# Performance work log

Hardware: AMD Instinct MI355X
Metric: run time of the kernel (lower is better)

The kernel has to match this reference:

```python
import jax, jax.numpy as jnp
import numpy as np

N_SPK, M_UTT, D_EMB = 1024, 32, 512


def setup_inputs() -> dict:
    key = jax.random.key(0)
    k0, = jax.random.split(key, 1)
    embeddings = jax.random.normal(k0, (N_SPK, M_UTT, D_EMB), dtype=jnp.float32)
    return {
        "embeddings": embeddings,
        "w": jnp.asarray(5.0, dtype=jnp.float32),
        "b": jnp.asarray(1.0, dtype=jnp.float32),
        "N": N_SPK,
        "M": M_UTT,
    }


def reference(embeddings, w, b, N, M):
    # embeddings: [N, M, D]
    centroids = embeddings.mean(axis=1)          # [N, D]
    sum_ = embeddings.sum(axis=1)                # [N, D]
    e_flat = embeddings.reshape(N * M, -1)       # [NM, D]
    cosine_sim = e_flat @ centroids.T            # [NM, N]

    # Exclusive-centroid diagonal overwrite (faithful to source, including
    # the operator precedence: c_j = sum_[j] - e[j,k] / (1 - M)):
    #   diag[j,k] = (sum_[j] - e[j,k]/(1-M)) . e[j,k]
    inv = 1.0 / (1.0 - M)
    diag = (jnp.einsum('nmd,nd->nm', embeddings, sum_)
            - inv * jnp.sum(embeddings * embeddings, axis=-1))  # [N, M]

    rows = jnp.arange(N * M)
    cols = jnp.repeat(jnp.arange(N), M)          # label layout: [0]*M, [1]*M, ...
    cosine_sim = cosine_sim.at[rows, cols].set(diag.reshape(-1))

    logits = w * cosine_sim + b                  # [NM, N]
    # cross_entropy with labels = cols, mean reduction
    logz = jax.nn.logsumexp(logits, axis=-1)     # [NM]
    loss = jnp.mean(logz - logits[rows, cols])
    return loss
```

## Files before the change

kernel.cpp:

```cpp
#include <hip/hip_runtime.h>

#define N_SPK 1024
#define M_UTT 32
#define D_EMB 512
#define NROWS (N_SPK * M_UTT)

#define NEG_INF (-__builtin_inff())
#define MARGIN 25.0f

using f32x4 = __attribute__((ext_vector_type(4))) float;


__global__ __launch_bounds__(256)
void prep_kernel(const float* __restrict__ e,
                 float* __restrict__ sumf, float* __restrict__ ssqA,
                 float* __restrict__ dgl, float* __restrict__ c2A,
                 const float* __restrict__ wp, const float* __restrict__ bp,
                 float* __restrict__ out, int* __restrict__ count,
                 int* __restrict__ doneCnt) {
    __shared__ float csum[4][D_EMB];
    __shared__ float c2red[4];
    const int n = blockIdx.x;
    const int wv = threadIdx.x >> 6, l = threadIdx.x & 63;

    if (n == 0 && threadIdx.x == 0) { out[0] = 0.f; *count = 0; *doneCnt = 0; }

    float xs[8][8];
    float ssq[8];
    float cacc[8];
#pragma unroll
    for (int j = 0; j < 8; ++j) cacc[j] = 0.f;

#pragma unroll
    for (int mi = 0; mi < 8; ++mi) {
        const int m = mi * 4 + wv;
        const size_t row = (size_t)n * M_UTT + m;
        const float* p = e + row * D_EMB + l * 8;
        float4 x0 = *(const float4*)p;
        float4 x1 = *(const float4*)(p + 4);
        xs[mi][0] = x0.x; xs[mi][1] = x0.y; xs[mi][2] = x0.z; xs[mi][3] = x0.w;
        xs[mi][4] = x1.x; xs[mi][5] = x1.y; xs[mi][6] = x1.z; xs[mi][7] = x1.w;
        float sq = 0.f;
#pragma unroll
        for (int j = 0; j < 8; ++j) {
            float x = xs[mi][j];
            cacc[j] += x;
            sq = __builtin_fmaf(x, x, sq);
        }
#pragma unroll
        for (int off = 32; off; off >>= 1) sq += __shfl_xor(sq, off);
        ssq[mi] = sq;
        if (l == 0) ssqA[row] = sq;
    }

#pragma unroll
    for (int j = 0; j < 8; ++j) csum[wv][l * 8 + j] = cacc[j];
    __syncthreads();
    float c2acc = 0.f;
    for (int d = threadIdx.x; d < D_EMB; d += 256) {
        float s = csum[0][d] + csum[1][d] + csum[2][d] + csum[3][d];
        csum[0][d] = s;
        sumf[(size_t)n * D_EMB + d] = s;
        float c = s * (1.0f / M_UTT);
        c2acc = __builtin_fmaf(c, c, c2acc);
    }
#pragma unroll
    for (int off = 32; off; off >>= 1) c2acc += __shfl_xor(c2acc, off);
    if (l == 0) c2red[wv] = c2acc;
    __syncthreads();
    if (threadIdx.x == 0)
        c2A[n] = (c2red[0] + c2red[1]) + (c2red[2] + c2red[3]);

    float sv[8];
#pragma unroll
    for (int j = 0; j < 8; ++j) sv[j] = csum[0][l * 8 + j];
    const float w = wp[0], bb = bp[0];
#pragma unroll
    for (int mi = 0; mi < 8; ++mi) {
        float dg = 0.f;
#pragma unroll
        for (int j = 0; j < 8; ++j) dg = __builtin_fmaf(xs[mi][j], sv[j], dg);
#pragma unroll
        for (int off = 32; off; off >>= 1) dg += __shfl_xor(dg, off);
        if (l == 0) {
            const size_t row = (size_t)n * M_UTT + mi * 4 + wv;
            dgl[row] = __builtin_fmaf(w, dg + ssq[mi] * (1.0f / 31.0f), bb);
        }
    }
}

__global__ __launch_bounds__(256)
void select_kernel(const float* __restrict__ ssqA, const float* __restrict__ dgl,
                   const float* __restrict__ c2A,
                   const float* __restrict__ wp, const float* __restrict__ bp,
                   int* __restrict__ count, int* __restrict__ active) {
    __shared__ float red[4];
    float m = 0.f;
#pragma unroll
    for (int i = 0; i < 4; ++i)
        m = fmaxf(m, c2A[threadIdx.x + i * 256]);
#pragma unroll
    for (int off = 32; off; off >>= 1) m = fmaxf(m, __shfl_xor(m, off));
    if ((threadIdx.x & 63) == 0) red[threadIdx.x >> 6] = m;
    __syncthreads();
    const float c2 = fmaxf(fmaxf(red[0], red[1]), fmaxf(red[2], red[3]));
    const float Cmax = __builtin_sqrtf(c2);

    const int row = blockIdx.x * 256 + threadIdx.x;
    const float bound = __builtin_fmaf(
        __builtin_fabsf(wp[0]) * __builtin_sqrtf(ssqA[row]), Cmax, bp[0]);
    if (dgl[row] - bound < MARGIN) {
        int slot = atomicAdd(count, 1);
        active[slot] = row;
    }
}

__global__ __launch_bounds__(64)
void active_kernel(const float* __restrict__ e, const float* __restrict__ sumf,
                   const float* __restrict__ dgl,
                   const int* __restrict__ count, const int* __restrict__ active,
                   const float* __restrict__ wp, const float* __restrict__ bp,
                   float2* __restrict__ pm16, int* __restrict__ doneCnt,
                   float* __restrict__ out) {
    __shared__ float er[D_EMB];
    __shared__ int lastFlag;
    const int tid = threadIdx.x;
    const int cnt = *count;
    if (cnt == 0) return;
    const float w = wp[0], bb = bp[0];

    const int g16 = blockIdx.x & 15;
    const int slot0 = blockIdx.x >> 4;
    const int gstride = gridDim.x >> 4;

    if (tid == 0) lastFlag = 0;
    int myItems = 0;

    for (int slot = slot0; slot < cnt; slot += gstride) {
        const int row = active[slot];
        __syncthreads();
#pragma unroll
        for (int i = 0; i < 8; ++i)
            er[tid + i * 64] = e[(size_t)row * D_EMB + tid + i * 64];
        __syncthreads();

        const int j = g16 * 64 + tid;
        const float* sp = sumf + (size_t)j * D_EMB;
        float d0 = 0.f, d1 = 0.f, d2 = 0.f, d3 = 0.f;
        for (int k = 0; k < D_EMB; k += 4) {
            float4 s4 = *(const float4*)(sp + k);
            d0 = __builtin_fmaf(er[k + 0], s4.x, d0);
            d1 = __builtin_fmaf(er[k + 1], s4.y, d1);
            d2 = __builtin_fmaf(er[k + 2], s4.z, d2);
            d3 = __builtin_fmaf(er[k + 3], s4.w, d3);
        }
        const float dot = (d0 + d1) + (d2 + d3);
        float lg = __builtin_fmaf(w, dot * (1.0f / M_UTT), bb);
        if (j == (row >> 5)) lg = dgl[row];

        float mx = lg;
#pragma unroll
        for (int off = 32; off; off >>= 1) mx = fmaxf(mx, __shfl_xor(mx, off));
        float ss = __expf(lg - mx);
#pragma unroll
        for (int off = 32; off; off >>= 1) ss += __shfl_xor(ss, off);
        if (tid == 0) {
            float2 v; v.x = mx; v.y = ss;
            __hip_atomic_store((unsigned long long*)&pm16[slot * 16 + g16],
                               __builtin_bit_cast(unsigned long long, v),
                               __ATOMIC_RELAXED, __HIP_MEMORY_SCOPE_AGENT);
        }
        ++myItems;
    }

    __syncthreads();
    if (tid == 0 && myItems > 0) {
        int old = __hip_atomic_fetch_add(doneCnt, myItems,
                                         __ATOMIC_ACQ_REL,
                                         __HIP_MEMORY_SCOPE_AGENT);
        if (old + myItems == cnt * 16) lastFlag = 1;
    }
    __syncthreads();

    if (lastFlag) {
        for (int slot = tid; slot < cnt; slot += 64) {
            float2 pm[4];
#pragma unroll
            for (int c = 0; c < 4; ++c) {
                float2 r0, r1, r2, r3;
                unsigned long long b0 = __hip_atomic_load(
                    (unsigned long long*)&pm16[slot * 16 + 4 * c + 0],
                    __ATOMIC_RELAXED, __HIP_MEMORY_SCOPE_AGENT);
                unsigned long long b1 = __hip_atomic_load(
                    (unsigned long long*)&pm16[slot * 16 + 4 * c + 1],
                    __ATOMIC_RELAXED, __HIP_MEMORY_SCOPE_AGENT);
                unsigned long long b2 = __hip_atomic_load(
                    (unsigned long long*)&pm16[slot * 16 + 4 * c + 2],
                    __ATOMIC_RELAXED, __HIP_MEMORY_SCOPE_AGENT);
                unsigned long long b3 = __hip_atomic_load(
                    (unsigned long long*)&pm16[slot * 16 + 4 * c + 3],
                    __ATOMIC_RELAXED, __HIP_MEMORY_SCOPE_AGENT);
                r0 = __builtin_bit_cast(float2, b0);
                r1 = __builtin_bit_cast(float2, b1);
                r2 = __builtin_bit_cast(float2, b2);
                r3 = __builtin_bit_cast(float2, b3);
                float M = fmaxf(fmaxf(r0.x, r1.x), fmaxf(r2.x, r3.x));
                float S = r0.y * __expf(r0.x - M)
                        + r1.y * __expf(r1.x - M)
                        + r2.y * __expf(r2.x - M)
                        + r3.y * __expf(r3.x - M);
                pm[c].x = M; pm[c].y = S;
            }
            float M = fmaxf(fmaxf(pm[0].x, pm[1].x), fmaxf(pm[2].x, pm[3].x));
            float S = pm[0].y * __expf(pm[0].x - M) + pm[1].y * __expf(pm[1].x - M)
                    + pm[2].y * __expf(pm[2].x - M) + pm[3].y * __expf(pm[3].x - M);
            float loss = M + __logf(S) - dgl[active[slot]];
            atomicAdd(out, loss * (1.0f / NROWS));
        }
    }
}


__global__ void centroid_kernel(const float* __restrict__ e,
                                float* __restrict__ cent) {
    int gid = blockIdx.x * 256 + threadIdx.x;
    int n = gid >> 9;
    int d = gid & 511;
    const float* p = e + ((size_t)n * M_UTT) * D_EMB + d;
    float s = 0.f;
#pragma unroll
    for (int m = 0; m < M_UTT; ++m) s += p[(size_t)m * D_EMB];
    cent[gid] = s * (1.0f / M_UTT);
}

__global__ void normsq_kernel(const float* __restrict__ e,
                              float* __restrict__ nsq) {
    int wv = threadIdx.x >> 6;
    int lane = threadIdx.x & 63;
    int row = blockIdx.x * 4 + wv;
    const float* p = e + (size_t)row * D_EMB + lane;
    float s = 0.f;
#pragma unroll
    for (int j = 0; j < 8; ++j) { float x = p[j * 64]; s += x * x; }
#pragma unroll
    for (int off = 32; off; off >>= 1) s += __shfl_xor(s, off);
    if (lane == 0) nsq[row] = s;
}

#define BR 64
#define BC 128
#define BK 16
#define TR 4
#define TC 8

__global__ __launch_bounds__(256, 2)
void ge2e_main(const float* __restrict__ e, const float* __restrict__ cent,
               const float* __restrict__ nsq, const float* __restrict__ wp,
               const float* __restrict__ bp, float* __restrict__ partials) {
    __shared__ float As[BK][BR];
    __shared__ float Bs[BK][BC];
    __shared__ float diagLs[BR];
    __shared__ float red[16];

    const int tid = threadIdx.x;
    const int tx = tid & 15;
    const int ty = tid >> 4;
    const int blk = blockIdx.x;
    const int r0 = blk * BR;

    const float w = *wp;
    const float bb = *bp;

    float m_run[TR], s_run[TR];
#pragma unroll
    for (int i = 0; i < TR; ++i) { m_run[i] = NEG_INF; s_run[i] = 0.f; }

    const int a_row = tid >> 2;
    const int a_k   = (tid & 3) * 4;
    const int b_col = tid >> 1;
    const int b_k   = (tid & 1) * 8;

    for (int ct = 0; ct < N_SPK / BC; ++ct) {
        const int c0 = ct * BC;
        float acc[TR][TC];
#pragma unroll
        for (int i = 0; i < TR; ++i)
#pragma unroll
            for (int j = 0; j < TC; ++j) acc[i][j] = 0.f;

        for (int kk = 0; kk < D_EMB; kk += BK) {
            __syncthreads();
            {
                float4 av = *(const float4*)(e + (size_t)(r0 + a_row) * D_EMB + kk + a_k);
                As[a_k + 0][a_row] = av.x;
                As[a_k + 1][a_row] = av.y;
                As[a_k + 2][a_row] = av.z;
                As[a_k + 3][a_row] = av.w;
            }
            {
                const float* bp0 = cent + (size_t)(c0 + b_col) * D_EMB + kk + b_k;
                float4 bv0 = *(const float4*)(bp0);
                float4 bv1 = *(const float4*)(bp0 + 4);
                Bs[b_k + 0][b_col] = bv0.x;
                Bs[b_k + 1][b_col] = bv0.y;
                Bs[b_k + 2][b_col] = bv0.z;
                Bs[b_k + 3][b_col] = bv0.w;
                Bs[b_k + 4][b_col] = bv1.x;
                Bs[b_k + 5][b_col] = bv1.y;
                Bs[b_k + 6][b_col] = bv1.z;
                Bs[b_k + 7][b_col] = bv1.w;
            }
            __syncthreads();

#pragma unroll
            for (int k = 0; k < BK; ++k) {
                float4 a4 = *(const float4*)&As[k][ty * TR];
                float4 b4a = *(const float4*)&Bs[k][tx * TC];
                float4 b4b = *(const float4*)&Bs[k][tx * TC + 4];
                float av[TR] = {a4.x, a4.y, a4.z, a4.w};
                float bv[TC] = {b4a.x, b4a.y, b4a.z, b4a.w,
                                b4b.x, b4b.y, b4b.z, b4b.w};
#pragma unroll
                for (int i = 0; i < TR; ++i)
#pragma unroll
                    for (int j = 0; j < TC; ++j)
                        acc[i][j] = __builtin_fmaf(av[i], bv[j], acc[i][j]);
            }
        }

#pragma unroll
        for (int i = 0; i < TR; ++i) {
            const int grow = r0 + ty * TR + i;
            const int dcol = grow >> 5;
            float lv[TC];
#pragma unroll
            for (int j = 0; j < TC; ++j) {
                const int gcol = c0 + tx * TC + j;
                float v = acc[i][j];
                float lg;
                if (gcol == dcol) {
                    lg = __builtin_fmaf(w, __builtin_fmaf(32.0f, v,
                             (1.0f / 31.0f) * nsq[grow]), bb);
                    diagLs[ty * TR + i] = lg;
                } else {
                    lg = __builtin_fmaf(w, v, bb);
                }
                lv[j] = lg;
            }
            float mx = lv[0];
#pragma unroll
            for (int j = 1; j < TC; ++j) mx = fmaxf(mx, lv[j]);
#pragma unroll
            for (int off = 8; off; off >>= 1) mx = fmaxf(mx, __shfl_xor(mx, off));
            float ss = 0.f;
#pragma unroll
            for (int j = 0; j < TC; ++j) ss += __expf(lv[j] - mx);
#pragma unroll
            for (int off = 8; off; off >>= 1) ss += __shfl_xor(ss, off);
            float nm = fmaxf(m_run[i], mx);
            s_run[i] = s_run[i] * __expf(m_run[i] - nm) + ss * __expf(mx - nm);
            m_run[i] = nm;
        }
    }

    __syncthreads();
    if (tx == 0) {
        float part = 0.f;
#pragma unroll
        for (int i = 0; i < TR; ++i) {
            const int lr = ty * TR + i;
            part += m_run[i] + __logf(s_run[i]) - diagLs[lr];
        }
        red[ty] = part;
    }
    __syncthreads();
    if (tid == 0) {
        float t = 0.f;
#pragma unroll
        for (int i = 0; i < 16; ++i) t += red[i];
        partials[blk] = t;
    }
}

__global__ void reduce_kernel(const float* __restrict__ partials,
                              float* __restrict__ out) {
    __shared__ float red[4];
    int tid = threadIdx.x;
    float v = partials[tid] + partials[tid + 256];
#pragma unroll
    for (int off = 32; off; off >>= 1) v += __shfl_xor(v, off);
    if ((tid & 63) == 0) red[tid >> 6] = v;
    __syncthreads();
    if (tid == 0)
        out[0] = (red[0] + red[1] + red[2] + red[3]) * (1.0f / NROWS);
}


extern "C" void kernel_launch(void* const* d_in, const int* in_sizes, int n_in,
                              void* d_out, int out_size, void* d_ws, size_t ws_size,
                              hipStream_t stream) {
    const float* e  = (const float*)d_in[0];
    const float* wp = (const float*)d_in[1];
    const float* bp = (const float*)d_in[2];
    float* out = (float*)d_out;

    const size_t NEED_FAST = 6688776ull;

    if (ws_size >= NEED_FAST) {
        char* base = (char*)d_ws;
        float*  sumf    = (float*) (base);
        float*  ssqA    = (float*) (base + 2097152ull);
        float*  dgl     = (float*) (base + 2228224ull);
        int*    active  = (int*)   (base + 2359296ull);
        float2* pm16    = (float2*)(base + 2490368ull);
        float*  c2A     = (float*) (base + 6684672ull);
        int*    count   = (int*)   (base + 6688768ull);
        int*    doneCnt = (int*)   (base + 6688772ull);

        prep_kernel<<<N_SPK, 256, 0, stream>>>(e, sumf, ssqA, dgl, c2A,
                                               wp, bp, out, count, doneCnt);
        select_kernel<<<NROWS / 256, 256, 0, stream>>>(ssqA, dgl, c2A,
                                                       wp, bp, count, active);
        active_kernel<<<1024, 64, 0, stream>>>(e, sumf, dgl, count, active,
                                               wp, bp, pm16, doneCnt, out);
    } else {
        float* ws = (float*)d_ws;
        float* cent     = ws;
        float* nsq      = ws + 524288;
        float* partials = ws + 524288 + 32768;

        centroid_kernel<<<N_SPK * D_EMB / 256, 256, 0, stream>>>(e, cent);
        normsq_kernel<<<NROWS / 4, 256, 0, stream>>>(e, nsq);
        ge2e_main<<<NROWS / BR, 256, 0, stream>>>(e, cent, nsq, wp, bp, partials);
        reduce_kernel<<<1, 256, 0, stream>>>(partials, out);
    }
}
```

Before: 118.0 us.

## Fuse row selection into active-row logsumexp kernel, indexing partials by row

Removes the separate select kernel. Each active-kernel block now computes the centroid-norm bound itself and ballots over a fixed range of 512 rows, then processes the active rows inline. Partial max/sum results are stored per row instead of per compacted slot. Completion is detected with a per-block counter rather than an item count. This drops one launch and the serial dependency on the global active count, but work is assigned statically by row position, so blocks can be imbalanced if active rows cluster.

Measured after the change: 130.9 us. 11.0% more time.

```diff
diff --git a/kernel.cpp b/kernel.cpp
--- a/kernel.cpp
+++ b/kernel.cpp
@@ -17,13 +17,13 @@
                  float* __restrict__ dgl, float* __restrict__ c2A,
                  const float* __restrict__ wp, const float* __restrict__ bp,
                  float* __restrict__ out, int* __restrict__ count,
-                 int* __restrict__ doneCnt) {
+                 int* __restrict__ blocksDone) {
     __shared__ float csum[4][D_EMB];
     __shared__ float c2red[4];
     const int n = blockIdx.x;
     const int wv = threadIdx.x >> 6, l = threadIdx.x & 63;
 
-    if (n == 0 && threadIdx.x == 0) { out[0] = 0.f; *count = 0; *doneCnt = 0; }
+    if (n == 0 && threadIdx.x == 0) { out[0] = 0.f; *count = 0; *blocksDone = 0; }
 
     float xs[8][8];
     float ssq[8];
@@ -89,132 +89,128 @@
     }
 }
 
-__global__ __launch_bounds__(256)
-void select_kernel(const float* __restrict__ ssqA, const float* __restrict__ dgl,
-                   const float* __restrict__ c2A,
-                   const float* __restrict__ wp, const float* __restrict__ bp,
-                   int* __restrict__ count, int* __restrict__ active) {
-    __shared__ float red[4];
-    float m = 0.f;
-#pragma unroll
-    for (int i = 0; i < 4; ++i)
-        m = fmaxf(m, c2A[threadIdx.x + i * 256]);
-#pragma unroll
-    for (int off = 32; off; off >>= 1) m = fmaxf(m, __shfl_xor(m, off));
-    if ((threadIdx.x & 63) == 0) red[threadIdx.x >> 6] = m;
-    __syncthreads();
-    const float c2 = fmaxf(fmaxf(red[0], red[1]), fmaxf(red[2], red[3]));
-    const float Cmax = __builtin_sqrtf(c2);
-
-    const int row = blockIdx.x * 256 + threadIdx.x;
-    const float bound = __builtin_fmaf(
-        __builtin_fabsf(wp[0]) * __builtin_sqrtf(ssqA[row]), Cmax, bp[0]);
-    if (dgl[row] - bound < MARGIN) {
-        int slot = atomicAdd(count, 1);
-        active[slot] = row;
-    }
-}
-
 __global__ __launch_bounds__(64)
-void active_kernel(const float* __restrict__ e, const float* __restrict__ sumf,
-                   const float* __restrict__ dgl,
-                   const int* __restrict__ count, const int* __restrict__ active,
-                   const float* __restrict__ wp, const float* __restrict__ bp,
-                   float2* __restrict__ pm16, int* __restrict__ doneCnt,
-                   float* __restrict__ out) {
+void act2_kernel(const float* __restrict__ e, const float* __restrict__ sumf,
+                 const float* __restrict__ ssqA, const float* __restrict__ dgl,
+                 const float* __restrict__ c2A,
+                 const float* __restrict__ wp, const float* __restrict__ bp,
+                 int* __restrict__ count, int* __restrict__ active,
+                 float2* __restrict__ pm16, int* __restrict__ blocksDone,
+                 float* __restrict__ out) {
     __shared__ float er[D_EMB];
     __shared__ int lastFlag;
     const int tid = threadIdx.x;
-    const int cnt = *count;
-    if (cnt == 0) return;
+    const int g16 = blockIdx.x & 15;
+    const int r0 = (blockIdx.x >> 4) * 512;
     const float w = wp[0], bb = bp[0];
 
-    const int g16 = blockIdx.x & 15;
-    const int slot0 = blockIdx.x >> 4;
-    const int gstride = gridDim.x >> 4;
-
-    if (tid == 0) lastFlag = 0;
-    int myItems = 0;
-
-    for (int slot = slot0; slot < cnt; slot += gstride) {
-        const int row = active[slot];
-        __syncthreads();
-#pragma unroll
-        for (int i = 0; i < 8; ++i)
-            er[tid + i * 64] = e[(size_t)row * D_EMB + tid + i * 64];
-        __syncthreads();
-
-        const int j = g16 * 64 + tid;
-        const float* sp = sumf + (size_t)j * D_EMB;
-        float d0 = 0.f, d1 = 0.f, d2 = 0.f, d3 = 0.f;
-        for (int k = 0; k < D_EMB; k += 4) {
-            float4 s4 = *(const float4*)(sp + k);
-            d0 = __builtin_fmaf(er[k + 0], s4.x, d0);
-            d1 = __builtin_fmaf(er[k + 1], s4.y, d1);
-            d2 = __builtin_fmaf(er[k + 2], s4.z, d2);
-            d3 = __builtin_fmaf(er[k + 3], s4.w, d3);
-        }
-        const float dot = (d0 + d1) + (d2 + d3);
-        float lg = __builtin_fmaf(w, dot * (1.0f / M_UTT), bb);
-        if (j == (row >> 5)) lg = dgl[row];
-
-        float mx = lg;
-#pragma unroll
-        for (int off = 32; off; off >>= 1) mx = fmaxf(mx, __shfl_xor(mx, off));
-        float ss = __expf(lg - mx);
-#pragma unroll
-        for (int off = 32; off; off >>= 1) ss += __shfl_xor(ss, off);
-        if (tid == 0) {
-            float2 v; v.x = mx; v.y = ss;
-            __hip_atomic_store((unsigned long long*)&pm16[slot * 16 + g16],
-                               __builtin_bit_cast(unsigned long long, v),
-                               __ATOMIC_RELAXED, __HIP_MEMORY_SCOPE_AGENT);
-        }
-        ++myItems;
-    }
-
-    __syncthreads();
-    if (tid == 0 && myItems > 0) {
-        int old = __hip_atomic_fetch_add(doneCnt, myItems,
-                                         __ATOMIC_ACQ_REL,
+    float m = 0.f;
+#pragma unroll
+    for (int i = 0; i < 16; ++i) m = fmaxf(m, c2A[tid + i * 64]);
+#pragma unroll
+    for (int off = 32; off; off >>= 1) m = fmaxf(m, __shfl_xor(m, off));
+    const float Cmax = __builtin_sqrtf(m);
+    const float aw = __builtin_fabsf(w);
+
+    for (int i = 0; i < 8; ++i) {
+        const int row = r0 + i * 64 + tid;
+        const float bound = __builtin_fmaf(
+            aw * __builtin_sqrtf(ssqA[row]), Cmax, bb);
+        unsigned long long mask = __ballot(dgl[row] - bound < MARGIN);
+        while (mask) {
+            const int bit = __builtin_ctzll(mask);
+            mask &= mask - 1;
+            const int srow = r0 + i * 64 + bit;
+
+            {
+                const float4* src = (const float4*)(e + (size_t)srow * D_EMB);
+                ((float4*)er)[tid * 2]     = src[tid * 2];
+                ((float4*)er)[tid * 2 + 1] = src[tid * 2 + 1];
+            }
+            __syncthreads();
+
+            const int j = g16 * 64 + tid;
+            const float* sp = sumf + (size_t)j * D_EMB;
+            float d0 = 0.f, d1 = 0.f, d2 = 0.f, d3 = 0.f;
+            for (int k = 0; k < D_EMB; k += 4) {
+                float4 s4 = *(const float4*)(sp + k);
+                d0 = __builtin_fmaf(er[k + 0], s4.x, d0);
+                d1 = __builtin_fmaf(er[k + 1], s4.y, d1);
+                d2 = __builtin_fmaf(er[k + 2], s4.z, d2);
+                d3 = __builtin_fmaf(er[k + 3], s4.w, d3);
+            }
+            const float dot = (d0 + d1) + (d2 + d3);
+            float lg = __builtin_fmaf(w, dot * (1.0f / M_UTT), bb);
+            if (j == (srow >> 5)) lg = dgl[srow];
+
+            float mx = lg;
+#pragma unroll
+            for (int off = 32; off; off >>= 1)
+                mx = fmaxf(mx, __shfl_xor(mx, off));
+            float ss = __expf(lg - mx);
+#pragma unroll
+            for (int off = 32; off; off >>= 1) ss += __shfl_xor(ss, off);
+
+            if (tid == 0) {
+                float2 v; v.x = mx; v.y = ss;
+                __hip_atomic_store(
+                    (unsigned long long*)&pm16[(size_t)srow * 16 + g16],
+                    __builtin_bit_cast(unsigned long long, v),
+                    __ATOMIC_RELAXED, __HIP_MEMORY_SCOPE_AGENT);
+                if (g16 == 0) {
+                    int slot = atomicAdd(count, 1);
+                    __hip_atomic_store(&active[slot], srow,
+                                       __ATOMIC_RELAXED,
+                                       __HIP_MEMORY_SCOPE_AGENT);
+                }
+            }
+            __syncthreads();
+        }
+    }
+
+    if (tid == 0) {
+        int old = __hip_atomic_fetch_add(blocksDone, 1, __ATOMIC_ACQ_REL,
                                          __HIP_MEMORY_SCOPE_AGENT);
-        if (old + myItems == cnt * 16) lastFlag = 1;
+        lastFlag = (old == (int)(gridDim.x) - 1);
     }
     __syncthreads();
 
     if (lastFlag) {
+        const int cnt = __hip_atomic_load(count, __ATOMIC_RELAXED,
+                                          __HIP_MEMORY_SCOPE_AGENT);
         for (int slot = tid; slot < cnt; slot += 64) {
+            const int row = __hip_atomic_load(&active[slot], __ATOMIC_RELAXED,
+                                              __HIP_MEMORY_SCOPE_AGENT);
             float2 pm[4];
 #pragma unroll
             for (int c = 0; c < 4; ++c) {
-                float2 r0, r1, r2, r3;
                 unsigned long long b0 = __hip_atomic_load(
-                    (unsigned long long*)&pm16[slot * 16 + 4 * c + 0],
+                    (unsigned long long*)&pm16[(size_t)row * 16 + 4 * c + 0],
                     __ATOMIC_RELAXED, __HIP_MEMORY_SCOPE_AGENT);
                 unsigned long long b1 = __hip_atomic_load(
-                    (unsigned long long*)&pm16[slot * 16 + 4 * c + 1],
+                    (unsigned long long*)&pm16[(size_t)row * 16 + 4 * c + 1],
                     __ATOMIC_RELAXED, __HIP_MEMORY_SCOPE_AGENT);
                 unsigned long long b2 = __hip_atomic_load(
-                    (unsigned long long*)&pm16[slot * 16 + 4 * c + 2],
+                    (unsigned long long*)&pm16[(size_t)row * 16 + 4 * c + 2],
                     __ATOMIC_RELAXED, __HIP_MEMORY_SCOPE_AGENT);
                 unsigned long long b3 = __hip_atomic_load(
-                    (unsigned long long*)&pm16[slot * 16 + 4 * c + 3],
+                    (unsigned long long*)&pm16[(size_t)row * 16 + 4 * c + 3],
                     __ATOMIC_RELAXED, __HIP_MEMORY_SCOPE_AGENT);
-                r0 = __builtin_bit_cast(float2, b0);
-                r1 = __builtin_bit_cast(float2, b1);
-                r2 = __builtin_bit_cast(float2, b2);
-                r3 = __builtin_bit_cast(float2, b3);
-                float M = fmaxf(fmaxf(r0.x, r1.x), fmaxf(r2.x, r3.x));
-                float S = r0.y * __expf(r0.x - M)
-                        + r1.y * __expf(r1.x - M)
-                        + r2.y * __expf(r2.x - M)
-                        + r3.y * __expf(r3.x - M);
+                float2 r0v = __builtin_bit_cast(float2, b0);
+                float2 r1v = __builtin_bit_cast(float2, b1);
+                float2 r2v = __builtin_bit_cast(float2, b2);
+                float2 r3v = __builtin_bit_cast(float2, b3);
+                float M = fmaxf(fmaxf(r0v.x, r1v.x), fmaxf(r2v.x, r3v.x));
+                float S = r0v.y * __expf(r0v.x - M)
+                        + r1v.y * __expf(r1v.x - M)
+                        + r2v.y * __expf(r2v.x - M)
+                        + r3v.y * __expf(r3v.x - M);
                 pm[c].x = M; pm[c].y = S;
             }
             float M = fmaxf(fmaxf(pm[0].x, pm[1].x), fmaxf(pm[2].x, pm[3].x));
             float S = pm[0].y * __expf(pm[0].x - M) + pm[1].y * __expf(pm[1].x - M)
                     + pm[2].y * __expf(pm[2].x - M) + pm[3].y * __expf(pm[3].x - M);
-            float loss = M + __logf(S) - dgl[active[slot]];
+            float loss = M + __logf(S) - dgl[row];
             atomicAdd(out, loss * (1.0f / NROWS));
         }
     }
@@ -408,21 +404,20 @@
 
     if (ws_size >= NEED_FAST) {
         char* base = (char*)d_ws;
-        float*  sumf    = (float*) (base);
-        float*  ssqA    = (float*) (base + 2097152ull);
-        float*  dgl     = (float*) (base + 2228224ull);
-        int*    active  = (int*)   (base + 2359296ull);
-        float2* pm16    = (float2*)(base + 2490368ull);
-        float*  c2A     = (float*) (base + 6684672ull);
-        int*    count   = (int*)   (base + 6688768ull);
-        int*    doneCnt = (int*)   (base + 6688772ull);
+        float*  sumf       = (float*) (base);
+        float*  ssqA       = (float*) (base + 2097152ull);
+        float*  dgl        = (float*) (base + 2228224ull);
+        int*    active     = (int*)   (base + 2359296ull);
+        float2* pm16       = (float2*)(base + 2490368ull);
+        float*  c2A        = (float*) (base + 6684672ull);
+        int*    count      = (int*)   (base + 6688768ull);
+        int*    blocksDone = (int*)   (base + 6688772ull);
 
         prep_kernel<<<N_SPK, 256, 0, stream>>>(e, sumf, ssqA, dgl, c2A,
-                                               wp, bp, out, count, doneCnt);
-        select_kernel<<<NROWS / 256, 256, 0, stream>>>(ssqA, dgl, c2A,
-                                                       wp, bp, count, active);
-        active_kernel<<<1024, 64, 0, stream>>>(e, sumf, dgl, count, active,
-                                               wp, bp, pm16, doneCnt, out);
+                                               wp, bp, out, count, blocksDone);
+        act2_kernel<<<1024, 64, 0, stream>>>(e, sumf, ssqA, dgl, c2A,
+                                             wp, bp, count, active, pm16,
+                                             blocksDone, out);
     } else {
         float* ws = (float*)d_ws;
         float* cent     = ws;
```
